# Optimization experiments

Hardware: AMD Instinct MI355X
Metric: run time of the kernel (lower is better)

Reference implementation:

```python
import jax, jax.numpy as jnp
import numpy as np

GROUP_SIZE = 64
IN_FEATURES = 4096
OUT_FEATURES = 4096
NUM_GROUPS = OUT_FEATURES * IN_FEATURES // GROUP_SIZE  # 262144
BYTES_PER_GROUP = GROUP_SIZE // 8 * 3  # 24
TOKENS = 8192


def block_dequantize_3bit(packed, scale, group_size=GROUP_SIZE):
    # packed: (G, bytes_per_group) int32 holding byte values 0..255
    p = packed.astype(jnp.uint8).astype(jnp.int32)  # byte semantics
    t = p.reshape(p.shape[0], -1, 3)  # (G, group_size//8, 3)
    b0, b1, b2 = t[..., 0], t[..., 1], t[..., 2]
    c0 = b0 & 7
    c1 = (b0 >> 3) & 7
    c2 = ((b0 >> 6) & 3) | ((b1 & 1) << 2)
    c3 = (b1 >> 1) & 7
    c4 = (b1 >> 4) & 7
    c5 = ((b1 >> 7) & 1) | ((b2 & 3) << 1)
    c6 = (b2 >> 2) & 7
    c7 = (b2 >> 5) & 7
    codes = jnp.stack([c0, c1, c2, c3, c4, c5, c6, c7], axis=-1)
    codes = codes.reshape(p.shape[0], group_size)  # (G, group_size)
    q = jnp.clip(codes - 3, -3, 3).astype(jnp.float32)
    return (q * scale.astype(jnp.float32)).reshape(-1)


def setup_inputs() -> dict:
    key = jax.random.key(0)
    k1, k2, k3, k4 = jax.random.split(key, 4)
    x = jax.random.normal(k1, (TOKENS, IN_FEATURES), dtype=jnp.float32)
    weight_q3 = jax.random.randint(k2, (NUM_GROUPS, BYTES_PER_GROUP), 0, 256, dtype=jnp.int32)
    weight_scale = jax.random.uniform(k3, (NUM_GROUPS, 1), dtype=jnp.float32)
    bias = jax.random.normal(k4, (OUT_FEATURES,), dtype=jnp.float32)
    return {"x": x, "weight_q3": weight_q3, "weight_scale": weight_scale, "bias": bias}


def reference(x, weight_q3, weight_scale, bias):
    w = block_dequantize_3bit(weight_q3, weight_scale).reshape(OUT_FEATURES, IN_FEATURES)
    out = jnp.einsum('ti,oi->to', x.astype(jnp.float32), w) + bias
    return out.astype(x.dtype)
```

## Files before the change

kernel.cpp:

```cpp
#include <hip/hip_runtime.h>

#define M_TOK 8192
#define N_OUT 4096
#define K_IN  4096
#define BK    64
#define NT    (K_IN / BK)

typedef __bf16 bf16;
typedef bf16  bf16x4  __attribute__((ext_vector_type(4)));
typedef bf16  bf16x8  __attribute__((ext_vector_type(8)));
typedef float floatx4 __attribute__((ext_vector_type(4)));

__device__ __forceinline__ bf16 dec_code(int c, float s) {
    int q = (c > 6 ? 6 : c) - 3;
    return (bf16)((float)q * s);
}

__device__ __forceinline__ void async_ld16(const bf16* g, const bf16* l) {
    __builtin_amdgcn_global_load_lds(
        (const __attribute__((address_space(1))) void*)g,
        (__attribute__((address_space(3))) void*)l,
        16, 0, 0);
}

__global__ __launch_bounds__(256)
void prep_kernel(const int* __restrict__ wq, const float* __restrict__ wscale,
                 const float* __restrict__ x,
                 bf16* __restrict__ W, bf16* __restrict__ xb)
{
    const int b = blockIdx.x;
    const int t = threadIdx.x;
    if (b < 2048) {
        int idx  = b * 256 + t;
        int g    = idx >> 1;
        int half = idx & 1;
        const int* wp = wq + (size_t)g * 24 + half * 12;
        int4 r0 = *(const int4*)(wp);
        int4 r1 = *(const int4*)(wp + 4);
        int4 r2 = *(const int4*)(wp + 8);
        float s = wscale[g];
        int by[12] = { r0.x, r0.y, r0.z, r0.w, r1.x, r1.y, r1.z, r1.w,
                       r2.x, r2.y, r2.z, r2.w };
        bf16* dst = W + (size_t)g * 64 + half * 32;
#pragma unroll
        for (int tri = 0; tri < 4; ++tri) {
            int b0 = by[tri * 3 + 0];
            int b1 = by[tri * 3 + 1];
            int b2 = by[tri * 3 + 2];
            bf16x8 h;
            h[0] = dec_code(b0 & 7, s);
            h[1] = dec_code((b0 >> 3) & 7, s);
            h[2] = dec_code(((b0 >> 6) & 3) | ((b1 & 1) << 2), s);
            h[3] = dec_code((b1 >> 1) & 7, s);
            h[4] = dec_code((b1 >> 4) & 7, s);
            h[5] = dec_code(((b1 >> 7) & 1) | ((b2 & 3) << 1), s);
            h[6] = dec_code((b2 >> 2) & 7, s);
            h[7] = dec_code((b2 >> 5) & 7, s);
            *(bf16x8*)(dst + tri * 8) = h;
        }
    } else {
        size_t i = ((size_t)(b - 2048) * 256 + t) * 8;
        float4 a = *(const float4*)(x + i);
        float4 c = *(const float4*)(x + i + 4);
        bf16x8 h = { (bf16)a.x, (bf16)a.y, (bf16)a.z, (bf16)a.w,
                     (bf16)c.x, (bf16)c.y, (bf16)c.z, (bf16)c.w };
        *(bf16x8*)(xb + i) = h;
    }
}

__global__ __launch_bounds__(512, 2)
void gemm_kernel(const bf16* __restrict__ A, const bf16* __restrict__ B,
                 const float* __restrict__ bias, float* __restrict__ out)
{
    __shared__ bf16 As[2][256][BK];
    __shared__ bf16 Bs[2][256][BK];

    const int t     = threadIdx.x;
    const int nBase = blockIdx.x * 256;
    const int mBase = blockIdx.y * 256;

    const int wave = t >> 6;
    const int lane = t & 63;
    const int quad = lane >> 4;
    const int r16  = lane & 15;
    const int wm   = wave >> 2;
    const int wn   = wave & 3;
    const int sw   = r16 & 7;

    const int rowInBlk = t >> 3;
    const int lc       = (t & 7) ^ (rowInBlk & 7);

    const bf16* aSrc = A + (size_t)(mBase + rowInBlk) * K_IN + lc * 8;
    const bf16* bSrc = B + (size_t)(nBase + rowInBlk) * K_IN + lc * 8;
    bf16* aLds0 = &As[0][0][0] + t * 8;
    bf16* bLds0 = &Bs[0][0][0] + t * 8;

#define STAGE_A(KT1, BUF, ROFF) \
    async_ld16(aSrc + (size_t)(ROFF) * K_IN + (size_t)(KT1) * BK, \
               aLds0 + (BUF) * 16384 + (ROFF) * BK)
#define STAGE_B(KT1, BUF, ROFF) \
    async_ld16(bSrc + (size_t)(ROFF) * K_IN + (size_t)(KT1) * BK, \
               bLds0 + (BUF) * 16384 + (ROFF) * BK)

    floatx4 acc[8][4];
#pragma unroll
    for (int i = 0; i < 8; ++i)
#pragma unroll
        for (int j = 0; j < 4; ++j)
            acc[i][j] = (floatx4){0.f, 0.f, 0.f, 0.f};

    STAGE_B(0, 0, 0);   STAGE_B(0, 0, 64);  STAGE_B(0, 0, 128); STAGE_B(0, 0, 192);
    STAGE_A(0, 0, 0);   STAGE_A(0, 0, 128); STAGE_A(0, 0, 64);  STAGE_A(0, 0, 192);

    bf16x8 bfr[2][4];

#define MFMA_PAIR(CB, M0) do {                                                  \
        bf16x8 af_[2][2];                                                       \
        _Pragma("unroll")                                                       \
        for (int ks = 0; ks < 2; ++ks)                                          \
            _Pragma("unroll")                                                   \
            for (int q = 0; q < 2; ++q)                                         \
                af_[ks][q] = *(const bf16x8*)(&As[CB][wm * 128 + ((M0) + q) * 16 + r16] \
                                                 [((ks * 4 + quad) ^ sw) * 8]); \
        __builtin_amdgcn_s_setprio(1);                                          \
        _Pragma("unroll")                                                       \
        for (int ks = 0; ks < 2; ++ks)                                          \
            _Pragma("unroll")                                                   \
            for (int q = 0; q < 2; ++q)                                         \
                _Pragma("unroll")                                               \
                for (int ni = 0; ni < 4; ++ni)                                  \
                    acc[(M0) + q][ni] = __builtin_amdgcn_mfma_f32_16x16x32_bf16(\
                        af_[ks][q], bfr[ks][ni], acc[(M0) + q][ni], 0, 0, 0);   \
        __builtin_amdgcn_s_setprio(0);                                          \
    } while (0)

    for (int kt = 0; kt < NT; ++kt) {
        const int  cb = kt & 1;
        const int  nb = cb ^ 1;
        const bool hn = (kt + 1 < NT);

        asm volatile("s_waitcnt vmcnt(2)\n\ts_barrier" ::: "memory");

        if (hn) {
            STAGE_B(kt + 1, nb, 0);   STAGE_B(kt + 1, nb, 64);
            STAGE_B(kt + 1, nb, 128); STAGE_B(kt + 1, nb, 192);
        }

#pragma unroll
        for (int ks = 0; ks < 2; ++ks)
#pragma unroll
            for (int ni = 0; ni < 4; ++ni)
                bfr[ks][ni] = *(const bf16x8*)(&Bs[cb][wn * 64 + ni * 16 + r16]
                                                  [((ks * 4 + quad) ^ sw) * 8]);

        MFMA_PAIR(cb, 0);

        if (hn) {
            STAGE_A(kt + 1, nb, 0);  STAGE_A(kt + 1, nb, 128);
            STAGE_A(kt + 1, nb, 64); STAGE_A(kt + 1, nb, 192);
        }

        MFMA_PAIR(cb, 2);

        if (hn) asm volatile("s_waitcnt vmcnt(8)\n\ts_barrier" ::: "memory");
        else    asm volatile("s_waitcnt vmcnt(0)\n\ts_barrier" ::: "memory");

        MFMA_PAIR(cb, 4);
        MFMA_PAIR(cb, 6);
    }

#undef MFMA_PAIR
#undef STAGE_A
#undef STAGE_B

    const int colBase = nBase + wn * 64;
#pragma unroll
    for (int ni = 0; ni < 4; ++ni) {
        int col  = colBase + ni * 16 + r16;
        float bv = bias[col];
#pragma unroll
        for (int mi = 0; mi < 8; ++mi) {
            int row0 = mBase + wm * 128 + mi * 16 + quad * 4;
#pragma unroll
            for (int r = 0; r < 4; ++r)
                out[(size_t)(row0 + r) * N_OUT + col] = acc[mi][ni][r] + bv;
        }
    }
}

__global__ __launch_bounds__(256, 2)
void linear3bit_fused(const float* __restrict__ x,
                      const int*   __restrict__ wq,
                      const float* __restrict__ wscale,
                      const float* __restrict__ bias,
                      float*       __restrict__ out)
{
    __shared__ bf16 As[128][BK];
    __shared__ bf16 Bs[128][BK];

    const int t     = threadIdx.x;
    const int mBase = blockIdx.y * 128;
    const int nBase = blockIdx.x * 128;

    const int wave = t >> 6;
    const int lane = t & 63;
    const int quad = lane >> 4;
    const int r16  = lane & 15;
    const int wm   = wave & 1;
    const int wn   = wave >> 1;

    floatx4 acc[4][4];
#pragma unroll
    for (int i = 0; i < 4; ++i)
#pragma unroll
        for (int j = 0; j < 4; ++j)
            acc[i][j] = (floatx4){0.f, 0.f, 0.f, 0.f};

    const int gl   = t >> 1;
    const int half = t & 1;
    const float* xBase = x + (size_t)mBase * K_IN;

    float4 aReg[8];
    int4   bReg[3];
    float  sReg;

    auto loadTile = [&](int kt) {
#pragma unroll
        for (int i = 0; i < 8; ++i) {
            int linear = i * 256 + t;
            int row    = linear >> 4;
            int c4     = (linear & 15) << 2;
            aReg[i] = *(const float4*)(xBase + (size_t)row * K_IN + kt * BK + c4);
        }
        size_t g = (size_t)(nBase + gl) * 64 + kt;
        const int* wp = wq + g * 24 + half * 12;
        bReg[0] = *(const int4*)(wp);
        bReg[1] = *(const int4*)(wp + 4);
        bReg[2] = *(const int4*)(wp + 8);
        sReg = wscale[g];
    };

    auto stage = [&]() {
#pragma unroll
        for (int i = 0; i < 8; ++i) {
            int linear = i * 256 + t;
            int row    = linear >> 4;
            int c4     = (linear & 15) << 2;
            float4 v = aReg[i];
            bf16x4 h = { (bf16)v.x, (bf16)v.y, (bf16)v.z, (bf16)v.w };
            *(bf16x4*)(&As[row][c4]) = h;
        }
        const float s = sReg;
        int by[12] = { bReg[0].x, bReg[0].y, bReg[0].z, bReg[0].w,
                       bReg[1].x, bReg[1].y, bReg[1].z, bReg[1].w,
                       bReg[2].x, bReg[2].y, bReg[2].z, bReg[2].w };
#pragma unroll
        for (int tri = 0; tri < 4; ++tri) {
            int b0 = by[tri * 3 + 0];
            int b1 = by[tri * 3 + 1];
            int b2 = by[tri * 3 + 2];
            bf16x8 h;
            h[0] = dec_code(b0 & 7, s);
            h[1] = dec_code((b0 >> 3) & 7, s);
            h[2] = dec_code(((b0 >> 6) & 3) | ((b1 & 1) << 2), s);
            h[3] = dec_code((b1 >> 1) & 7, s);
            h[4] = dec_code((b1 >> 4) & 7, s);
            h[5] = dec_code(((b1 >> 7) & 1) | ((b2 & 3) << 1), s);
            h[6] = dec_code((b2 >> 2) & 7, s);
            h[7] = dec_code((b2 >> 5) & 7, s);
            *(bf16x8*)(&Bs[gl][half * 32 + tri * 8]) = h;
        }
    };

    auto compute = [&]() {
#pragma unroll
        for (int ks = 0; ks < 2; ++ks) {
            bf16x8 af[4], bfr[4];
#pragma unroll
            for (int mi = 0; mi < 4; ++mi)
                af[mi] = *(const bf16x8*)(&As[wm * 64 + mi * 16 + r16][ks * 32 + quad * 8]);
#pragma unroll
            for (int ni = 0; ni < 4; ++ni)
                bfr[ni] = *(const bf16x8*)(&Bs[wn * 64 + ni * 16 + r16][ks * 32 + quad * 8]);
#pragma unroll
            for (int mi = 0; mi < 4; ++mi)
#pragma unroll
                for (int ni = 0; ni < 4; ++ni)
                    acc[mi][ni] = __builtin_amdgcn_mfma_f32_16x16x32_bf16(
                        af[mi], bfr[ni], acc[mi][ni], 0, 0, 0);
        }
    };

    loadTile(0);
    for (int kt = 0; kt < NT; ++kt) {
        __syncthreads();
        stage();
        __syncthreads();
        if (kt + 1 < NT) loadTile(kt + 1);
        compute();
    }

    const int colBase = nBase + wn * 64;
#pragma unroll
    for (int ni = 0; ni < 4; ++ni) {
        int col  = colBase + ni * 16 + r16;
        float bv = bias[col];
#pragma unroll
        for (int mi = 0; mi < 4; ++mi) {
            int row0 = mBase + wm * 64 + mi * 16 + quad * 4;
#pragma unroll
            for (int r = 0; r < 4; ++r)
                out[(size_t)(row0 + r) * N_OUT + col] = acc[mi][ni][r] + bv;
        }
    }
}

extern "C" void kernel_launch(void* const* d_in, const int* in_sizes, int n_in,
                              void* d_out, int out_size, void* d_ws, size_t ws_size,
                              hipStream_t stream) {
    const float* x      = (const float*)d_in[0];
    const int*   wq     = (const int*)d_in[1];
    const float* wscale = (const float*)d_in[2];
    const float* bias   = (const float*)d_in[3];
    float*       out    = (float*)d_out;

    const size_t wBytes  = (size_t)N_OUT * K_IN * sizeof(bf16);
    const size_t xBytes  = (size_t)M_TOK * K_IN * sizeof(bf16);

    if (ws_size >= wBytes + xBytes) {
        bf16* Wb = (bf16*)d_ws;
        bf16* Xb = (bf16*)((char*)d_ws + wBytes);
        prep_kernel<<<2048 + 16384, 256, 0, stream>>>(wq, wscale, x, Wb, Xb);
        dim3 grid(N_OUT / 256, M_TOK / 256);
        gemm_kernel<<<grid, dim3(512), 0, stream>>>(Xb, Wb, bias, out);
    } else {
        dim3 grid(N_OUT / 128, M_TOK / 128);
        linear3bit_fused<<<grid, dim3(256), 0, stream>>>(x, wq, wscale, bias, out);
    }
}
```

Before: 538.4 us.

## Restructure GEMM main loop into four barrier-separated phases with interleaved staging

Reorganizes each K-iteration into four phases. Each phase loads A/B fragments from LDS, issues part of the next tile's async global-to-LDS copies, synchronizes, and then runs a 4x2 MFMA cluster. This is a ping-pong style schedule meant to overlap LDS reads, global loads and MFMA work more evenly across waves. It adds extra barriers per iteration and relies on carefully tuned vmcnt waits, which risks stalls or hazards on buffer reuse.

```diff
diff --git a/kernel.cpp b/kernel.cpp
--- a/kernel.cpp
+++ b/kernel.cpp
@@ -109,67 +109,85 @@
         for (int j = 0; j < 4; ++j)
             acc[i][j] = (floatx4){0.f, 0.f, 0.f, 0.f};
 
+    bf16x8 afr[2][4];
+    bf16x8 bfr[2][4];
+
+#define LOAD_A(CB, MH) do {                                                     \
+        _Pragma("unroll") for (int ks = 0; ks < 2; ++ks)                        \
+        _Pragma("unroll") for (int q = 0; q < 4; ++q)                           \
+            afr[ks][q] = *(const bf16x8*)(                                      \
+                &As[CB][wm * 128 + ((MH) * 4 + q) * 16 + r16]                   \
+                      [((ks * 4 + quad) ^ sw) * 8]);                            \
+    } while (0)
+#define LOAD_B(CB, NJ) do {                                                     \
+        _Pragma("unroll") for (int ks = 0; ks < 2; ++ks)                        \
+        _Pragma("unroll") for (int j = 0; j < 2; ++j)                           \
+            bfr[ks][(NJ) * 2 + j] = *(const bf16x8*)(                           \
+                &Bs[CB][wn * 64 + ((NJ) * 2 + j) * 16 + r16]                    \
+                      [((ks * 4 + quad) ^ sw) * 8]);                            \
+    } while (0)
+
+#define CLUSTER(MOFF, NOFF) do {                                                \
+        __builtin_amdgcn_s_setprio(1);                                          \
+        _Pragma("unroll") for (int ks = 0; ks < 2; ++ks)                        \
+        _Pragma("unroll") for (int q = 0; q < 4; ++q)                           \
+        _Pragma("unroll") for (int j = 0; j < 2; ++j)                           \
+            acc[(MOFF) + q][(NOFF) + j] =                                       \
+                __builtin_amdgcn_mfma_f32_16x16x32_bf16(                        \
+                    afr[ks][q], bfr[ks][(NOFF) + j],                            \
+                    acc[(MOFF) + q][(NOFF) + j], 0, 0, 0);                      \
+        __builtin_amdgcn_s_setprio(0);                                          \
+    } while (0)
+
+#define PH_SYNC() do {                                                          \
+        asm volatile("s_barrier\n\ts_waitcnt lgkmcnt(0)" ::: "memory");         \
+        __builtin_amdgcn_sched_barrier(0);                                      \
+    } while (0)
+#define PH_END() asm volatile("s_barrier" ::: "memory")
+
     STAGE_B(0, 0, 0);   STAGE_B(0, 0, 64);  STAGE_B(0, 0, 128); STAGE_B(0, 0, 192);
     STAGE_A(0, 0, 0);   STAGE_A(0, 0, 128); STAGE_A(0, 0, 64);  STAGE_A(0, 0, 192);
-
-    bf16x8 bfr[2][4];
-
-#define MFMA_PAIR(CB, M0) do {                                                  \
-        bf16x8 af_[2][2];                                                       \
-        _Pragma("unroll")                                                       \
-        for (int ks = 0; ks < 2; ++ks)                                          \
-            _Pragma("unroll")                                                   \
-            for (int q = 0; q < 2; ++q)                                         \
-                af_[ks][q] = *(const bf16x8*)(&As[CB][wm * 128 + ((M0) + q) * 16 + r16] \
-                                                 [((ks * 4 + quad) ^ sw) * 8]); \
-        __builtin_amdgcn_s_setprio(1);                                          \
-        _Pragma("unroll")                                                       \
-        for (int ks = 0; ks < 2; ++ks)                                          \
-            _Pragma("unroll")                                                   \
-            for (int q = 0; q < 2; ++q)                                         \
-                _Pragma("unroll")                                               \
-                for (int ni = 0; ni < 4; ++ni)                                  \
-                    acc[(M0) + q][ni] = __builtin_amdgcn_mfma_f32_16x16x32_bf16(\
-                        af_[ks][q], bfr[ks][ni], acc[(M0) + q][ni], 0, 0, 0);   \
-        __builtin_amdgcn_s_setprio(0);                                          \
-    } while (0)
+    asm volatile("s_waitcnt vmcnt(2)" ::: "memory");
+    asm volatile("s_barrier" ::: "memory");
 
     for (int kt = 0; kt < NT; ++kt) {
         const int  cb = kt & 1;
         const int  nb = cb ^ 1;
         const bool hn = (kt + 1 < NT);
 
-        asm volatile("s_waitcnt vmcnt(2)\n\ts_barrier" ::: "memory");
-
-        if (hn) {
-            STAGE_B(kt + 1, nb, 0);   STAGE_B(kt + 1, nb, 64);
-            STAGE_B(kt + 1, nb, 128); STAGE_B(kt + 1, nb, 192);
-        }
-
-#pragma unroll
-        for (int ks = 0; ks < 2; ++ks)
-#pragma unroll
-            for (int ni = 0; ni < 4; ++ni)
-                bfr[ks][ni] = *(const bf16x8*)(&Bs[cb][wn * 64 + ni * 16 + r16]
-                                                  [((ks * 4 + quad) ^ sw) * 8]);
-
-        MFMA_PAIR(cb, 0);
-
-        if (hn) {
-            STAGE_A(kt + 1, nb, 0);  STAGE_A(kt + 1, nb, 128);
-            STAGE_A(kt + 1, nb, 64); STAGE_A(kt + 1, nb, 192);
-        }
-
-        MFMA_PAIR(cb, 2);
-
-        if (hn) asm volatile("s_waitcnt vmcnt(8)\n\ts_barrier" ::: "memory");
-        else    asm volatile("s_waitcnt vmcnt(0)\n\ts_barrier" ::: "memory");
-
-        MFMA_PAIR(cb, 4);
-        MFMA_PAIR(cb, 6);
-    }
-
-#undef MFMA_PAIR
+        LOAD_A(cb, 0);
+        LOAD_B(cb, 0);
+        if (hn) { STAGE_B(kt + 1, nb, 0); STAGE_B(kt + 1, nb, 64); }
+        PH_SYNC();
+        CLUSTER(0, 0);
+        PH_END();
+
+        LOAD_B(cb, 1);
+        if (hn) { STAGE_B(kt + 1, nb, 128); STAGE_B(kt + 1, nb, 192); }
+        PH_SYNC();
+        CLUSTER(0, 2);
+        if (hn) asm volatile("s_waitcnt vmcnt(4)" ::: "memory");
+        else    asm volatile("s_waitcnt vmcnt(0)" ::: "memory");
+        PH_END();
+
+        LOAD_A(cb, 1);
+        if (hn) { STAGE_A(kt + 1, nb, 0); STAGE_A(kt + 1, nb, 128); }
+        PH_SYNC();
+        CLUSTER(4, 0);
+        PH_END();
+
+        if (hn) { STAGE_A(kt + 1, nb, 64); STAGE_A(kt + 1, nb, 192); }
+        PH_SYNC();
+        CLUSTER(4, 2);
+        if (hn) asm volatile("s_waitcnt vmcnt(2)" ::: "memory");
+        PH_END();
+    }
+
+#undef PH_END
+#undef PH_SYNC
+#undef CLUSTER
+#undef LOAD_B
+#undef LOAD_A
 #undef STAGE_A
 #undef STAGE_B
 
```

Result: faster. 470.2 us, median of 2 (-12.7%).
